# Performance work log

Measured on AMD Instinct MI355X. Metric: run time of the kernel, lower is better.

The kernel has to match this reference:

```python
import jax, jax.numpy as jnp
import numpy as np

B, T, H, NH = 4, 1024, 1024, 16
HS = H // NH
FF = 4 * H
EPS = 1e-5


def setup_inputs() -> dict:
    key = jax.random.key(0)
    ks = jax.random.split(key, 12)
    s = 0.02
    inp = {
        "x": jax.random.normal(ks[0], (B, T, H), jnp.float32),
        # attention projections, stored as [in, out] so y = x @ W + b
        "Wq": jax.random.normal(ks[1], (H, H), jnp.float32) * s,
        "bq": jnp.zeros((H,), jnp.float32),
        "Wk": jax.random.normal(ks[2], (H, H), jnp.float32) * s,
        "bk": jnp.zeros((H,), jnp.float32),
        "Wv": jax.random.normal(ks[3], (H, H), jnp.float32) * s,
        "bv": jnp.zeros((H,), jnp.float32),
        "Wo": jax.random.normal(ks[4], (H, H), jnp.float32) * s,
        "bo": jnp.zeros((H,), jnp.float32),
        # layernorms
        "ln1_w": jnp.ones((H,), jnp.float32),
        "ln1_b": jnp.zeros((H,), jnp.float32),
        "ln2_w": jnp.ones((H,), jnp.float32),
        "ln2_b": jnp.zeros((H,), jnp.float32),
        # MLP
        "Wfc": jax.random.normal(ks[5], (H, FF), jnp.float32) * s,
        "bfc": jnp.zeros((FF,), jnp.float32),
        "Wpr": jax.random.normal(ks[6], (FF, H), jnp.float32) * s,
        "bpr": jnp.zeros((H,), jnp.float32),
    }
    return inp


def _layernorm(x, w, b):
    mu = jnp.mean(x, axis=-1, keepdims=True)
    var = jnp.mean(jnp.square(x - mu), axis=-1, keepdims=True)
    return (x - mu) * jax.lax.rsqrt(var + EPS) * w + b


def _rope(x):
    # x: [B, nh, T, hs]; interleaved-pair RoPE, base 10000
    half = HS // 2
    inv_freq = 1.0 / (10000.0 ** (jnp.arange(half, dtype=jnp.float32) / half))
    ang = jnp.arange(T, dtype=jnp.float32)[:, None] * inv_freq[None, :]  # [T, half]
    cos, sin = jnp.cos(ang), jnp.sin(ang)
    xr = x.reshape(*x.shape[:-1], half, 2)
    x0, x1 = xr[..., 0], xr[..., 1]
    r0 = x0 * cos - x1 * sin
    r1 = x0 * sin + x1 * cos
    return jnp.stack([r0, r1], axis=-1).reshape(x.shape)


def _block(x, Wq, bq, Wk, bk, Wv, bv, Wo, bo, ln1_w, ln1_b, ln2_w, ln2_b, Wfc, bfc, Wpr, bpr):
    # --- attention sub-block ---
    h1 = _layernorm(x, ln1_w, ln1_b)
    q = (h1 @ Wq + bq).reshape(B, T, NH, HS).transpose(0, 2, 1, 3)  # [B,nh,T,hs]
    k = (h1 @ Wk + bk).reshape(B, T, NH, HS).transpose(0, 2, 1, 3)
    v = (h1 @ Wv + bv).reshape(B, T, NH, HS).transpose(0, 2, 1, 3)
    q, k = _rope(q), _rope(k)
    scores = jnp.einsum('bhqd,bhkd->bhqk', q, k) / jnp.sqrt(jnp.float32(HS))
    attn = jax.nn.softmax(scores, axis=-1)
    # NOTE: original applies the causal mask AFTER softmax (multiplicative, no renorm)
    causal = jnp.tril(jnp.ones((T, T), jnp.float32))[None, None]
    attn = attn * causal
    out = jnp.einsum('bhqk,bhkd->bhqd', attn, v)
    out = out.transpose(0, 2, 1, 3).reshape(B, T, H)
    x = x + (out @ Wo + bo)
    # --- MLP sub-block ---
    h2 = _layernorm(x, ln2_w, ln2_b)
    m = jax.nn.gelu(h2 @ Wfc + bfc, approximate=False)
    x = x + (m @ Wpr + bpr)
    return x


def reference(x, Wq, bq, Wk, bk, Wv, bv, Wo, bo, ln1_w, ln1_b, ln2_w, ln2_b, Wfc, bfc, Wpr, bpr):
    return _block(x, Wq, bq, Wk, bk, Wv, bv, Wo, bo, ln1_w, ln1_b, ln2_w, ln2_b, Wfc, bfc, Wpr, bpr)
```

## Files before the change

### kernel.cpp

```cpp
#include <hip/hip_runtime.h>
#include <hip/hip_bf16.h>

typedef unsigned short u16;
typedef __attribute__((ext_vector_type(8))) short bf16x8;
typedef __attribute__((ext_vector_type(4))) float f32x4;
typedef __attribute__((ext_vector_type(4))) unsigned short u16x4;

#define B_  4
#define T_  1024
#define H_  1024
#define NH_ 16
#define HS_ 64
#define FF_ 4096
#define M_  (B_*T_)
#define QKV_S 3072

__device__ __forceinline__ u16 f2bf(float f){
  union { float f; unsigned u; } v; v.f = f;
  unsigned r = v.u + 0x7fffu + ((v.u >> 16) & 1u);
  return (u16)(r >> 16);
}
__device__ __forceinline__ float bf2f(u16 h){
  union { unsigned u; float f; } v; v.u = ((unsigned)h) << 16;
  return v.f;
}
__device__ __forceinline__ unsigned pack2bf(float a, float b){
  __hip_bfloat162 h = __float22bfloat162_rn(make_float2(a, b));
  union { __hip_bfloat162 h; unsigned u; } c; c.h = h;
  return c.u;
}

__device__ __forceinline__ void gload_lds16(const void* g, void* l){
  __builtin_amdgcn_global_load_lds(
      (const __attribute__((address_space(1))) unsigned int*)g,
      (__attribute__((address_space(3))) unsigned int*)l,
      16, 0, 0);
}

__global__ __launch_bounds__(256) void transpose_cvt(const float* __restrict__ W,
                                                     u16* __restrict__ Wt, int K, int N)
{
  __shared__ u16 tile[64][68];
  const int k0 = blockIdx.y * 64, n0 = blockIdx.x * 64;
  const int tid = threadIdx.x;
  #pragma unroll
  for (int it = 0; it < 4; ++it){
    int ci = tid + it * 256;
    int kr = ci >> 4, nc = ci & 15;
    float4 f = *(const float4*)(W + (size_t)(k0 + kr) * N + n0 + nc * 4);
    tile[kr][nc*4+0] = f2bf(f.x);
    tile[kr][nc*4+1] = f2bf(f.y);
    tile[kr][nc*4+2] = f2bf(f.z);
    tile[kr][nc*4+3] = f2bf(f.w);
  }
  __syncthreads();
  #pragma unroll
  for (int it = 0; it < 4; ++it){
    int co = tid + it * 256;
    int nr = co >> 4, kc = co & 15;
    u16x4 o;
    o[0] = tile[kc*4+0][nr];
    o[1] = tile[kc*4+1][nr];
    o[2] = tile[kc*4+2][nr];
    o[3] = tile[kc*4+3][nr];
    *(u16x4*)(Wt + (size_t)(n0 + nr) * K + k0 + kc * 4) = o;
  }
}

__global__ __launch_bounds__(256) void vtrans_k(const u16* __restrict__ qkv,
                                                u16* __restrict__ vtg)
{
  __shared__ u16 tile[64][72];
  const int bh = blockIdx.y, tt = blockIdx.x * 64;
  const int b = bh >> 4, h = bh & 15;
  const size_t src = (size_t)b * T_ * QKV_S + h * HS_ + 2048;
  const int tid = threadIdx.x;
  #pragma unroll
  for (int it = 0; it < 2; ++it){
    int ci = tid + it * 256;
    int r = ci >> 3, c = ci & 7;
    bf16x8 vvv = *(const bf16x8*)(qkv + src + (size_t)(tt + r) * QKV_S + c * 8);
    *(bf16x8*)&tile[r][c * 8] = vvv;
  }
  __syncthreads();
  #pragma unroll
  for (int it = 0; it < 2; ++it){
    int co = tid + it * 256;
    int d = co >> 3, c = co & 7;
    bf16x8 ov;
    #pragma unroll
    for (int j = 0; j < 8; ++j) ov[j] = (short)tile[c * 8 + j][d];
    *(bf16x8*)(vtg + (size_t)bh * HS_ * T_ + (size_t)d * T_ + tt + c * 8) = ov;
  }
}

__global__ void concat3_k(const float* __restrict__ a, const float* __restrict__ b,
                          const float* __restrict__ c, float* __restrict__ o){
  int i = blockIdx.x * 256 + threadIdx.x;
  if (i >= QKV_S) return;
  o[i] = (i < 1024) ? a[i] : (i < 2048) ? b[i - 1024] : c[i - 2048];
}

__global__ void rope_table_k(float* __restrict__ tab){
  int i = blockIdx.x * blockDim.x + threadIdx.x;
  if (i >= T_ * 32) return;
  int t = i >> 5, f = i & 31;
  float inv = powf(10000.0f, -(float)f * (1.0f / 32.0f));
  float ang = (float)t * inv;
  tab[i*2+0] = cosf(ang);
  tab[i*2+1] = sinf(ang);
}

__global__ void rope_apply_k(u16* __restrict__ qkv, const float* __restrict__ tab){
  int i = blockIdx.x * blockDim.x + threadIdx.x;
  if (i >= B_*T_*NH_*32) return;
  int pr = i & 31;
  int nh = (i >> 5) & (NH_ - 1);
  int bt = i >> 9;
  int t  = bt & (T_ - 1);
  size_t idx = (size_t)bt * QKV_S + nh * HS_ + pr * 2;
  float c = tab[(t*32 + pr)*2], s = tab[(t*32 + pr)*2 + 1];
  const float qs = 0.125f * 1.44269504f;
  {
    float x0 = bf2f(qkv[idx]), x1 = bf2f(qkv[idx+1]);
    qkv[idx]   = f2bf((x0 * c - x1 * s) * qs);
    qkv[idx+1] = f2bf((x0 * s + x1 * c) * qs);
  }
  {
    float x0 = bf2f(qkv[idx+1024]), x1 = bf2f(qkv[idx+1025]);
    qkv[idx+1024] = f2bf(x0 * c - x1 * s);
    qkv[idx+1025] = f2bf(x0 * s + x1 * c);
  }
}

__global__ __launch_bounds__(256) void ln_kernel(const float* __restrict__ x,
    const float* __restrict__ w, const float* __restrict__ bgain,
    u16* __restrict__ out)
{
  const int row = blockIdx.x;
  const int t = threadIdx.x;
  float4 vv = ((const float4*)(x + (size_t)row * H_))[t];
  float s  = vv.x + vv.y + vv.z + vv.w;
  float s2 = vv.x*vv.x + vv.y*vv.y + vv.z*vv.z + vv.w*vv.w;
  #pragma unroll
  for (int mm = 1; mm < 64; mm <<= 1){ s += __shfl_xor(s, mm); s2 += __shfl_xor(s2, mm); }
  __shared__ float red[8];
  int wid = t >> 6;
  if ((t & 63) == 0){ red[wid] = s; red[4 + wid] = s2; }
  __syncthreads();
  s  = red[0] + red[1] + red[2] + red[3];
  s2 = red[4] + red[5] + red[6] + red[7];
  float mu  = s * (1.0f / H_);
  float var = s2 * (1.0f / H_) - mu * mu;
  float rin = rsqrtf(var + 1e-5f);
  float4 wv = ((const float4*)w)[t];
  float4 bv = ((const float4*)bgain)[t];
  u16x4 ov;
  ov[0] = f2bf((vv.x - mu) * rin * wv.x + bv.x);
  ov[1] = f2bf((vv.y - mu) * rin * wv.y + bv.y);
  ov[2] = f2bf((vv.z - mu) * rin * wv.z + bv.z);
  ov[3] = f2bf((vv.w - mu) * rin * wv.w + bv.w);
  ((u16x4*)(out + (size_t)row * H_))[t] = ov;
}

template<int EPI, int RING>
__global__ __launch_bounds__(512) void gemm_kernel(
    const u16* __restrict__ A, const u16* __restrict__ Bt,
    const float* __restrict__ bias, const float* __restrict__ res,
    void* __restrict__ Cout, int M, int N, int K)
{
  __shared__ __attribute__((aligned(16))) u16 As[RING][128 * 32];
  __shared__ __attribute__((aligned(16))) u16 Bs[RING][128 * 32];
  const int tid  = threadIdx.x;
  const int lane = tid & 63;
  const int wid  = tid >> 6;
  const int wm = wid >> 2, wn = wid & 3;
  const int lrow = lane & 15, lkg = lane >> 4;

  const int gx  = gridDim.x;
  const int nwg = gx * gridDim.y;
  const int wg  = blockIdx.y * gx + blockIdx.x;
  const int nx  = nwg >> 3;
  const int swz = (wg & 7) * nx + (wg >> 3);
  const int m0 = (swz / gx) * 128, n0 = (swz % gx) * 128;

  const int srow = tid >> 2;
  const int sdc  = tid & 3;
  const int scs  = sdc ^ ((srow >> 1) & 3);

  const u16* Arow = A  + (size_t)(m0 + srow) * K + scs * 8;
  const u16* Brow = Bt + (size_t)(n0 + srow) * K + scs * 8;
  const int dd = (srow * 4 + sdc) * 8;

  f32x4 acc[4][2] = {};
  const int NT = K >> 5;
  constexpr int DIST = RING - 1;

  #pragma unroll
  for (int s = 0; s < DIST; ++s){
    gload_lds16(Arow + (s << 5), &As[s][dd]);
    gload_lds16(Brow + (s << 5), &Bs[s][dd]);
  }

  int rs = 0, wsl = DIST;
  for (int t = 0; t < NT; ++t){
    int cnt = NT - 1 - t; if (cnt > DIST - 1) cnt = DIST - 1;
    if (cnt >= 4)      asm volatile("s_waitcnt vmcnt(8)" ::: "memory");
    else if (cnt == 3) asm volatile("s_waitcnt vmcnt(6)" ::: "memory");
    else if (cnt == 2) asm volatile("s_waitcnt vmcnt(4)" ::: "memory");
    else if (cnt == 1) asm volatile("s_waitcnt vmcnt(2)" ::: "memory");
    else               asm volatile("s_waitcnt vmcnt(0)" ::: "memory");
    __builtin_amdgcn_s_barrier();

    const u16* Asc = As[rs];
    const u16* Bsc = Bs[rs];
    rs = (rs + 1 == RING) ? 0 : rs + 1;

    bf16x8 af[4], bfr[2];
    #pragma unroll
    for (int mi = 0; mi < 4; ++mi){
      int r = wm*64 + mi*16 + lrow;
      af[mi] = *(const bf16x8*)&Asc[(r*4 + (lkg ^ ((r >> 1) & 3))) * 8];
    }
    #pragma unroll
    for (int ni = 0; ni < 2; ++ni){
      int r = wn*32 + ni*16 + lrow;
      bfr[ni] = *(const bf16x8*)&Bsc[(r*4 + (lkg ^ ((r >> 1) & 3))) * 8];
    }
    __builtin_amdgcn_sched_barrier(0);

    if (t + DIST < NT){
      int k0 = (t + DIST) << 5;
      gload_lds16(Arow + k0, &As[wsl][dd]);
      gload_lds16(Brow + k0, &Bs[wsl][dd]);
    }
    wsl = (wsl + 1 == RING) ? 0 : wsl + 1;

    #pragma unroll
    for (int mi = 0; mi < 4; ++mi)
      #pragma unroll
      for (int ni = 0; ni < 2; ++ni)
        acc[mi][ni] = __builtin_amdgcn_mfma_f32_16x16x32_bf16(af[mi], bfr[ni], acc[mi][ni], 0, 0, 0);
  }

  #pragma unroll
  for (int mi = 0; mi < 4; ++mi){
    #pragma unroll
    for (int ni = 0; ni < 2; ++ni){
      int col = n0 + wn*32 + ni*16 + lrow;
      float bv = bias[col];
      #pragma unroll
      for (int r = 0; r < 4; ++r){
        int row = m0 + wm*64 + mi*16 + lkg*4 + r;
        float v = acc[mi][ni][r] + bv;
        if (EPI == 1){
          v = 0.5f * v * (1.0f + erff(v * 0.70710678118f));
        }
        if (EPI == 2){
          ((float*)Cout)[(size_t)row * N + col] = v + res[(size_t)row * N + col];
        } else {
          ((u16*)Cout)[(size_t)row * N + col] = f2bf(v);
        }
      }
    }
  }
}

__global__ __launch_bounds__(512, 4) void attn_kernel(
    const u16* __restrict__ qkv, const u16* __restrict__ vtg,
    u16* __restrict__ out)
{
  __shared__ u16 K_lds[3][64 * 64];
  __shared__ u16 VT_lds[3][64 * 64];
  __shared__ u16 P_lds[8][16 * 64];
  const int tid = threadIdx.x, lane = tid & 63, w = tid >> 6;
  const int lrow = lane & 15, lkg = lane >> 4;
  const int q0 = blockIdx.x * 128;
  const int bh = blockIdx.y, b = bh >> 4, h = bh & 15;
  const size_t baseq  = (size_t)b * T_ * QKV_S + h * HS_;
  const size_t basek  = baseq + 1024;
  const size_t basevt = (size_t)bh * HS_ * T_;
  const size_t baseo  = (size_t)b * T_ * H_ + h * HS_;
  const int qg = q0 + w * 16 + lrow;

  bf16x8 qa[2];
  {
    const u16* qp = qkv + baseq + (size_t)qg * QKV_S + lkg * 8;
    qa[0] = *(const bf16x8*)qp;
    qa[1] = *(const bf16x8*)(qp + 32);
  }

  const int r0 = tid >> 3, c0 = tid & 7, g0 = c0 ^ (r0 & 7);
  const u16* kap = qkv + basek + (size_t)r0 * QKV_S + g0 * 8;
  const u16* vap = vtg + basevt + (size_t)r0 * T_ + g0 * 8;
  const int kd = tid * 8;

  f32x4 o[4] = {};
  float mrun = -1e30f, lrun = 0.f;

  #pragma unroll
  for (int s = 0; s < 2; ++s){
    gload_lds16(kap + (size_t)s * 64 * QKV_S, &K_lds[s][kd]);
    gload_lds16(vap + s * 64,                 &VT_lds[s][kd]);
  }

  int rs = 0, wsl = 2;
  for (int t = 0; t < 16; ++t){
    const int kt = t << 6;
    if (t < 15) asm volatile("s_waitcnt vmcnt(2)" ::: "memory");
    else        asm volatile("s_waitcnt vmcnt(0)" ::: "memory");
    __builtin_amdgcn_s_barrier();
    __builtin_amdgcn_sched_barrier(0);

    if (t + 2 < 16){
      gload_lds16(kap + (size_t)(t + 2) * 64 * QKV_S, &K_lds[wsl][kd]);
      gload_lds16(vap + (t + 2) * 64,                 &VT_lds[wsl][kd]);
    }
    wsl = (wsl + 1 == 3) ? 0 : wsl + 1;

    const u16* Kc  = K_lds[rs];
    const u16* VTc = VT_lds[rs];
    rs = (rs + 1 == 3) ? 0 : rs + 1;

    f32x4 s[4];
    __builtin_amdgcn_s_setprio(1);
    #pragma unroll
    for (int mi = 0; mi < 4; ++mi){
      f32x4 c = {};
      #pragma unroll
      for (int ss = 0; ss < 2; ++ss){
        int r = mi * 16 + lrow;
        int off = r * 128 + (((ss * 4 + lkg) ^ (r & 7)) * 16);
        bf16x8 kb = *(const bf16x8*)((const char*)Kc + off);
        c = __builtin_amdgcn_mfma_f32_16x16x32_bf16(kb, qa[ss], c, 0, 0, 0);
      }
      s[mi] = c;
    }
    __builtin_amdgcn_s_setprio(0);

    float mt = fmaxf(fmaxf(fmaxf(s[0][0], s[0][1]), fmaxf(s[0][2], s[0][3])),
                     fmaxf(fmaxf(s[1][0], s[1][1]), fmaxf(s[1][2], s[1][3])));
    mt = fmaxf(mt, fmaxf(fmaxf(fmaxf(s[2][0], s[2][1]), fmaxf(s[2][2], s[2][3])),
                         fmaxf(fmaxf(s[3][0], s[3][1]), fmaxf(s[3][2], s[3][3]))));
    mt = fmaxf(mt, __shfl_xor(mt, 16));
    mt = fmaxf(mt, __shfl_xor(mt, 32));
    if (!__all(mt <= mrun + 8.f)){
      float mnew = fmaxf(mrun, mt);
      float fsc = exp2f(mrun - mnew);
      lrun *= fsc;
      #pragma unroll
      for (int nf = 0; nf < 4; ++nf){
        #pragma unroll
        for (int r = 0; r < 4; ++r) o[nf][r] *= fsc;
      }
      mrun = mnew;
    }

    float p[16];
    float ls = 0.f;
    #pragma unroll
    for (int mi = 0; mi < 4; ++mi){
      #pragma unroll
      for (int r = 0; r < 4; ++r){
        int key = kt + mi * 16 + lkg * 4 + r;
        float pv = exp2f(s[mi][r] - mrun);
        ls += pv;
        p[mi * 4 + r] = (key <= qg) ? pv : 0.f;
      }
    }
    ls += __shfl_xor(ls, 16);
    ls += __shfl_xor(ls, 32);
    lrun += ls;

    if (kt <= q0 + w * 16 + 15){
      char* pbase = (char*)&P_lds[w][0];
      const int rx = (lrow & 7) << 4;
      #pragma unroll
      for (int mi = 0; mi < 4; ++mi){
        uint2 pk;
        pk.x = pack2bf(p[mi*4+0], p[mi*4+1]);
        pk.y = pack2bf(p[mi*4+2], p[mi*4+3]);
        *(uint2*)(pbase + (lrow * 128 + ((mi * 32 + lkg * 8) ^ rx))) = pk;
      }
      __builtin_amdgcn_s_setprio(1);
      #pragma unroll
      for (int ss = 0; ss < 2; ++ss){
        bf16x8 pb = *(const bf16x8*)(pbase + (lrow * 128 + ((ss * 64 + lkg * 16) ^ rx)));
        #pragma unroll
        for (int nfd = 0; nfd < 4; ++nfd){
          int d = nfd * 16 + lrow;
          int off = d * 128 + (((ss * 4 + lkg) ^ (d & 7)) * 16);
          bf16x8 vb = *(const bf16x8*)((const char*)VTc + off);
          o[nfd] = __builtin_amdgcn_mfma_f32_16x16x32_bf16(vb, pb, o[nfd], 0, 0, 0);
        }
      }
      __builtin_amdgcn_s_setprio(0);
    }
  }

  float rl = 1.0f / lrun;
  #pragma unroll
  for (int nfd = 0; nfd < 4; ++nfd){
    uint2 ov;
    ov.x = pack2bf(o[nfd][0] * rl, o[nfd][1] * rl);
    ov.y = pack2bf(o[nfd][2] * rl, o[nfd][3] * rl);
    *(uint2*)(out + baseo + (size_t)qg * H_ + nfd * 16 + lkg * 4) = ov;
  }
}

extern "C" void kernel_launch(void* const* d_in, const int* in_sizes, int n_in,
                              void* d_out, int out_size, void* d_ws, size_t ws_size,
                              hipStream_t stream)
{
  (void)in_sizes; (void)n_in; (void)out_size; (void)ws_size;
  const float* x    = (const float*)d_in[0];
  const float* Wq   = (const float*)d_in[1];
  const float* bq   = (const float*)d_in[2];
  const float* Wk   = (const float*)d_in[3];
  const float* bk   = (const float*)d_in[4];
  const float* Wv   = (const float*)d_in[5];
  const float* bv   = (const float*)d_in[6];
  const float* Wo   = (const float*)d_in[7];
  const float* bo   = (const float*)d_in[8];
  const float* ln1w = (const float*)d_in[9];
  const float* ln1b = (const float*)d_in[10];
  const float* ln2w = (const float*)d_in[11];
  const float* ln2b = (const float*)d_in[12];
  const float* Wfc  = (const float*)d_in[13];
  const float* bfc  = (const float*)d_in[14];
  const float* Wpr  = (const float*)d_in[15];
  const float* bpr  = (const float*)d_in[16];

  char* ws = (char*)d_ws;
  u16*  WqkvT = (u16*)(ws + ((size_t) 0 << 20));
  u16*  WoT   = (u16*)(ws + ((size_t) 6 << 20));
  u16*  WfcT  = (u16*)(ws + ((size_t) 8 << 20));
  u16*  WprT  = (u16*)(ws + ((size_t)16 << 20));
  u16*  h1    = (u16*)(ws + ((size_t)24 << 20));
  u16*  qkvb  = (u16*)(ws + ((size_t)32 << 20));
  float* x1   = (float*)(ws + ((size_t)32 << 20));
  u16*  h2    = (u16*)(ws + ((size_t)48 << 20));
  float* bqkv = (float*)(ws + ((size_t)56 << 20));
  float* rtab = (float*)(ws + ((size_t)56 << 20) + (64 << 10));
  u16*  vtg   = (u16*)(ws + ((size_t)57 << 20));
  u16*  mb    = (u16*)(ws + ((size_t)56 << 20));
  u16*  attnout = h1;

  dim3 blk(256);
  dim3 gblk(512);

  transpose_cvt<<<dim3(H_/64,  H_/64),  blk, 0, stream>>>(Wq,  WqkvT,                 H_,  H_);
  transpose_cvt<<<dim3(H_/64,  H_/64),  blk, 0, stream>>>(Wk,  WqkvT + (size_t)1024*1024, H_,  H_);
  transpose_cvt<<<dim3(H_/64,  H_/64),  blk, 0, stream>>>(Wv,  WqkvT + (size_t)2048*1024, H_,  H_);
  transpose_cvt<<<dim3(H_/64,  H_/64),  blk, 0, stream>>>(Wo,  WoT,  H_,  H_);
  transpose_cvt<<<dim3(FF_/64, H_/64),  blk, 0, stream>>>(Wfc, WfcT, H_,  FF_);
  transpose_cvt<<<dim3(H_/64,  FF_/64), blk, 0, stream>>>(Wpr, WprT, FF_, H_);
  concat3_k<<<dim3((QKV_S+255)/256), blk, 0, stream>>>(bq, bk, bv, bqkv);
  rope_table_k<<<dim3((T_*32)/256), blk, 0, stream>>>(rtab);

  ln_kernel<<<dim3(M_), blk, 0, stream>>>(x, ln1w, ln1b, h1);
  gemm_kernel<0,3><<<dim3(QKV_S/128, M_/128), gblk, 0, stream>>>(h1, WqkvT, bqkv, nullptr, qkvb, M_, QKV_S, H_);
  rope_apply_k<<<dim3((B_*T_*NH_*32)/256), blk, 0, stream>>>(qkvb, rtab);
  vtrans_k<<<dim3(T_/64, B_*NH_), blk, 0, stream>>>(qkvb, vtg);
  attn_kernel<<<dim3(T_/128, B_*NH_), dim3(512), 0, stream>>>(qkvb, vtg, attnout);
  gemm_kernel<2,6><<<dim3(H_/128, M_/128), gblk, 0, stream>>>(attnout, WoT, bo, x, x1, M_, H_, H_);
  ln_kernel<<<dim3(M_), blk, 0, stream>>>(x1, ln2w, ln2b, h2);
  gemm_kernel<1,3><<<dim3(FF_/128, M_/128), gblk, 0, stream>>>(h2, WfcT, bfc, nullptr, mb, M_, FF_, H_);
  gemm_kernel<2,6><<<dim3(H_/128, M_/128), gblk, 0, stream>>>(mb, WprT, bpr, x1, (float*)d_out, M_, H_, FF_);
}
```

Before: 263.3 us.

## Merge small prep launches, precompute LDS offsets, use tanh-approx GELU

The four QKV/O weight transposes now run as one launch over a z-dimension, and the bias concat and RoPE table kernels are merged into one launch, cutting per-launch overhead. The GEMM hoists the swizzled LDS fragment offsets out of the K loop into registers. The exact erf GELU in the FC epilogue is replaced by the tanh approximation, computed as x*sigmoid via exp2. That is a numerical approximation of the reference's exact GELU and may slightly change results.

```diff
diff --git a/kernel.cpp b/kernel.cpp
--- a/kernel.cpp
+++ b/kernel.cpp
@@ -37,12 +37,11 @@
       16, 0, 0);
 }
 
-__global__ __launch_bounds__(256) void transpose_cvt(const float* __restrict__ W,
-                                                     u16* __restrict__ Wt, int K, int N)
+__device__ __forceinline__ void trans_tile(const float* __restrict__ W,
+                                           u16* __restrict__ Wt, int K, int N,
+                                           int k0, int n0, int tid)
 {
   __shared__ u16 tile[64][68];
-  const int k0 = blockIdx.y * 64, n0 = blockIdx.x * 64;
-  const int tid = threadIdx.x;
   #pragma unroll
   for (int it = 0; it < 4; ++it){
     int ci = tid + it * 256;
@@ -67,6 +66,23 @@
   }
 }
 
+__global__ __launch_bounds__(256) void trans_qkvo_k(
+    const float* __restrict__ Wq, const float* __restrict__ Wk,
+    const float* __restrict__ Wv, const float* __restrict__ Wo,
+    u16* __restrict__ WqkvT, u16* __restrict__ WoT)
+{
+  const int z = blockIdx.z;
+  const float* src = (z == 0) ? Wq : (z == 1) ? Wk : (z == 2) ? Wv : Wo;
+  u16* dst = (z == 3) ? WoT : (WqkvT + (size_t)z * 1024 * 1024);
+  trans_tile(src, dst, H_, H_, blockIdx.y * 64, blockIdx.x * 64, threadIdx.x);
+}
+
+__global__ __launch_bounds__(256) void transpose_cvt(const float* __restrict__ W,
+                                                     u16* __restrict__ Wt, int K, int N)
+{
+  trans_tile(W, Wt, K, N, blockIdx.y * 64, blockIdx.x * 64, threadIdx.x);
+}
+
 __global__ __launch_bounds__(256) void vtrans_k(const u16* __restrict__ qkv,
                                                 u16* __restrict__ vtg)
 {
@@ -94,21 +110,22 @@
   }
 }
 
-__global__ void concat3_k(const float* __restrict__ a, const float* __restrict__ b,
-                          const float* __restrict__ c, float* __restrict__ o){
+__global__ void prep_small_k(const float* __restrict__ a, const float* __restrict__ b,
+                             const float* __restrict__ c, float* __restrict__ o,
+                             float* __restrict__ tab){
   int i = blockIdx.x * 256 + threadIdx.x;
-  if (i >= QKV_S) return;
-  o[i] = (i < 1024) ? a[i] : (i < 2048) ? b[i - 1024] : c[i - 2048];
-}
-
-__global__ void rope_table_k(float* __restrict__ tab){
-  int i = blockIdx.x * blockDim.x + threadIdx.x;
-  if (i >= T_ * 32) return;
-  int t = i >> 5, f = i & 31;
-  float inv = powf(10000.0f, -(float)f * (1.0f / 32.0f));
-  float ang = (float)t * inv;
-  tab[i*2+0] = cosf(ang);
-  tab[i*2+1] = sinf(ang);
+  if (i < QKV_S){
+    o[i] = (i < 1024) ? a[i] : (i < 2048) ? b[i - 1024] : c[i - 2048];
+  } else {
+    int j = i - QKV_S;
+    if (j < T_ * 32){
+      int t = j >> 5, f = j & 31;
+      float inv = powf(10000.0f, -(float)f * (1.0f / 32.0f));
+      float ang = (float)t * inv;
+      tab[j*2+0] = cosf(ang);
+      tab[j*2+1] = sinf(ang);
+    }
+  }
 }
 
 __global__ void rope_apply_k(u16* __restrict__ qkv, const float* __restrict__ tab){
@@ -192,6 +209,18 @@
   const u16* Brow = Bt + (size_t)(n0 + srow) * K + scs * 8;
   const int dd = (srow * 4 + sdc) * 8;
 
+  int aoff[4], boff[2];
+  #pragma unroll
+  for (int mi = 0; mi < 4; ++mi){
+    int r = wm*64 + mi*16 + lrow;
+    aoff[mi] = (r*4 + (lkg ^ ((r >> 1) & 3))) * 16;
+  }
+  #pragma unroll
+  for (int ni = 0; ni < 2; ++ni){
+    int r = wn*32 + ni*16 + lrow;
+    boff[ni] = (r*4 + (lkg ^ ((r >> 1) & 3))) * 16;
+  }
+
   f32x4 acc[4][2] = {};
   const int NT = K >> 5;
   constexpr int DIST = RING - 1;
@@ -212,21 +241,17 @@
     else               asm volatile("s_waitcnt vmcnt(0)" ::: "memory");
     __builtin_amdgcn_s_barrier();
 
-    const u16* Asc = As[rs];
-    const u16* Bsc = Bs[rs];
+    const char* Ab = (const char*)&As[rs][0];
+    const char* Bb = (const char*)&Bs[rs][0];
     rs = (rs + 1 == RING) ? 0 : rs + 1;
 
     bf16x8 af[4], bfr[2];
     #pragma unroll
-    for (int mi = 0; mi < 4; ++mi){
-      int r = wm*64 + mi*16 + lrow;
-      af[mi] = *(const bf16x8*)&Asc[(r*4 + (lkg ^ ((r >> 1) & 3))) * 8];
-    }
-    #pragma unroll
-    for (int ni = 0; ni < 2; ++ni){
-      int r = wn*32 + ni*16 + lrow;
-      bfr[ni] = *(const bf16x8*)&Bsc[(r*4 + (lkg ^ ((r >> 1) & 3))) * 8];
-    }
+    for (int mi = 0; mi < 4; ++mi)
+      af[mi] = *(const bf16x8*)(Ab + aoff[mi]);
+    #pragma unroll
+    for (int ni = 0; ni < 2; ++ni)
+      bfr[ni] = *(const bf16x8*)(Bb + boff[ni]);
     __builtin_amdgcn_sched_barrier(0);
 
     if (t + DIST < NT){
@@ -254,7 +279,9 @@
         int row = m0 + wm*64 + mi*16 + lkg*4 + r;
         float v = acc[mi][ni][r] + bv;
         if (EPI == 1){
-          v = 0.5f * v * (1.0f + erff(v * 0.70710678118f));
+          float u = 0.7978845608f * v + 0.0356774081f * v * v * v;
+          float e = exp2f(u * 2.8853900818f);
+          v = v - v / (e + 1.0f);
         }
         if (EPI == 2){
           ((float*)Cout)[(size_t)row * N + col] = v + res[(size_t)row * N + col];
@@ -449,14 +476,10 @@
   dim3 blk(256);
   dim3 gblk(512);
 
-  transpose_cvt<<<dim3(H_/64,  H_/64),  blk, 0, stream>>>(Wq,  WqkvT,                 H_,  H_);
-  transpose_cvt<<<dim3(H_/64,  H_/64),  blk, 0, stream>>>(Wk,  WqkvT + (size_t)1024*1024, H_,  H_);
-  transpose_cvt<<<dim3(H_/64,  H_/64),  blk, 0, stream>>>(Wv,  WqkvT + (size_t)2048*1024, H_,  H_);
-  transpose_cvt<<<dim3(H_/64,  H_/64),  blk, 0, stream>>>(Wo,  WoT,  H_,  H_);
+  trans_qkvo_k<<<dim3(H_/64, H_/64, 4), blk, 0, stream>>>(Wq, Wk, Wv, Wo, WqkvT, WoT);
   transpose_cvt<<<dim3(FF_/64, H_/64),  blk, 0, stream>>>(Wfc, WfcT, H_,  FF_);
   transpose_cvt<<<dim3(H_/64,  FF_/64), blk, 0, stream>>>(Wpr, WprT, FF_, H_);
-  concat3_k<<<dim3((QKV_S+255)/256), blk, 0, stream>>>(bq, bk, bv, bqkv);
-  rope_table_k<<<dim3((T_*32)/256), blk, 0, stream>>>(rtab);
+  prep_small_k<<<dim3((QKV_S + T_*32 + 255)/256), blk, 0, stream>>>(bq, bk, bv, bqkv, rtab);
 
   ln_kernel<<<dim3(M_), blk, 0, stream>>>(x, ln1w, ln1b, h1);
   gemm_kernel<0,3><<<dim3(QKV_S/128, M_/128), gblk, 0, stream>>>(h1, WqkvT, bqkv, nullptr, qkvb, M_, QKV_S, H_);
```

Result: faster. 254.0 us (-3.5%).
